# Performance work log

Measured on AMD Instinct MI355X. Metric: run time of the kernel, lower is better.

Reference implementation:

```python
import jax, jax.numpy as jnp
import numpy as np

N_NODES = 100000
EMB_DIM = 64
HIDDEN = 8
OUT_DIM = 16
NUM_HEADS = 3
B = 1024
E_RAND = 3200000


def setup_inputs() -> dict:
    key = jax.random.key(0)
    ks = jax.random.split(key, 12)
    src = jax.random.randint(ks[0], (E_RAND,), 0, N_NODES, dtype=jnp.int32)
    dst = jax.random.randint(ks[1], (E_RAND,), 0, N_NODES, dtype=jnp.int32)
    loop = jnp.arange(N_NODES, dtype=jnp.int32)
    src = jnp.concatenate([src, loop])
    dst = jnp.concatenate([dst, loop])
    # multi-hot query indicator, ~50 items per query, guarantee >=1 item
    queries = (jax.random.uniform(ks[2], (B, N_NODES)) < 5e-4).astype(jnp.float32)
    queries = queries.at[:, 0].set(1.0)
    pos_items = jax.random.randint(ks[3], (B,), 0, N_NODES, dtype=jnp.int32)
    neg_items = jax.random.randint(ks[4], (B,), 0, N_NODES, dtype=jnp.int32)
    embedding = jax.random.normal(ks[5], (N_NODES, EMB_DIM), dtype=jnp.float32) * 0.1
    # GAT layer 1: NUM_HEADS heads, in=64 -> out=8 per head (concat)
    W1 = jax.random.normal(ks[6], (NUM_HEADS, EMB_DIM, HIDDEN), dtype=jnp.float32) * 0.1
    a1 = jax.random.normal(ks[7], (NUM_HEADS, 2 * HIDDEN), dtype=jnp.float32) * 0.1
    # GAT layer 2: 1 head, in=24 -> out=16
    W2 = jax.random.normal(ks[8], (NUM_HEADS * HIDDEN, OUT_DIM), dtype=jnp.float32) * 0.1
    a2 = jax.random.normal(ks[9], (2 * OUT_DIM,), dtype=jnp.float32) * 0.1
    return {"queries": queries, "pos_items": pos_items, "neg_items": neg_items,
            "embedding": embedding, "W1": W1, "a1": a1, "W2": W2, "a2": a2,
            "src": src, "dst": dst}


def gat_layer(h, W, a, src, dst, n_nodes):
    # h: [N, in], W: [H, in, o], a: [H, 2o]; returns [N, H, o]
    o = W.shape[-1]
    z = jnp.einsum('nd,hdo->nho', h, W)            # [N,H,o]
    zs, zd = z[src], z[dst]                         # [E,H,o]
    e = jax.nn.leaky_relu(
        jnp.einsum('eho,ho->eh', zs, a[:, :o]) +
        jnp.einsum('eho,ho->eh', zd, a[:, o:]), 0.01)  # [E,H]
    m = jax.ops.segment_max(e, dst, num_segments=n_nodes)       # [N,H]
    alpha = jnp.exp(e - m[dst])                                  # [E,H]
    denom = jax.ops.segment_sum(alpha, dst, num_segments=n_nodes)
    num = jax.ops.segment_sum(alpha[:, :, None] * zs, dst, num_segments=n_nodes)
    return num / denom[:, :, None]


def gat_forward(embedding, W1, a1, W2, a2, src, dst):
    n = embedding.shape[0]
    h1 = gat_layer(embedding, W1, a1, src, dst, n)       # [N,H,hid]
    h1 = jax.nn.elu(h1.reshape(n, -1))                   # [N,H*hid]
    h2 = gat_layer(h1, W2[None], a2[None], src, dst, n)  # [N,1,out]
    return h2[:, 0]                                      # [N,out]


def reference(queries, pos_items, neg_items, embedding, W1, a1, W2, a2, src, dst):
    item_embeds = gat_forward(embedding, W1, a1, W2, a2, src, dst)  # [N,16]
    item_cnt = jnp.sum(queries, axis=1)                              # [B]
    query_embeds = jnp.matmul(queries, item_embeds) / item_cnt[:, None]
    pos_embed = item_embeds[pos_items]
    neg_embed = item_embeds[neg_items]
    return (query_embeds, pos_embed, neg_embed)
```

## Files before the change

### kernel.cpp

```cpp
#include <hip/hip_runtime.h>
#include <hip/hip_fp16.h>

#define NH 3
#define HID 8
#define C1 24
#define C2 16
#define BSH 5
#define BNODES 32
#define NBMAX 3200
#define SCAP 1792
#define PCHUNK 32768
#define AZS 32

__device__ inline float2 cvt2(unsigned u) {
    __half2 h;
    *reinterpret_cast<unsigned*>(&h) = u;
    return __half22float2(h);
}

__global__ __launch_bounds__(256) void k_z1(
    const float* __restrict__ emb, const float* __restrict__ W1g,
    const float* __restrict__ a1g, __half* __restrict__ az1h,
    float4* __restrict__ f1d, int* __restrict__ bcnt, int NB, int N) {
    __shared__ float sW[NH * 64 * HID];
    __shared__ float sa[NH * 2 * HID];
    for (int i = threadIdx.x; i < NH * 64 * HID; i += blockDim.x) sW[i] = W1g[i];
    for (int i = threadIdx.x; i < NH * 2 * HID; i += blockDim.x) sa[i] = a1g[i];
    int n = blockIdx.x * blockDim.x + threadIdx.x;
    if (n < NB) bcnt[n] = 0;
    __syncthreads();
    if (n >= N) return;
    float e[64];
    const float4* ep = (const float4*)(emb + (size_t)n * 64);
#pragma unroll
    for (int i = 0; i < 16; ++i) {
        float4 v = ep[i];
        e[4*i+0] = v.x; e[4*i+1] = v.y; e[4*i+2] = v.z; e[4*i+3] = v.w;
    }
    float z[C1];
#pragma unroll
    for (int c = 0; c < C1; ++c) z[c] = 0.f;
    for (int d = 0; d < 64; ++d) {
        float ed = e[d];
#pragma unroll
        for (int h = 0; h < NH; ++h) {
            const float4* wp = (const float4*)&sW[(h * 64 + d) * HID];
            float4 w0 = wp[0], w1 = wp[1];
            z[h*HID+0] += ed * w0.x; z[h*HID+1] += ed * w0.y;
            z[h*HID+2] += ed * w0.z; z[h*HID+3] += ed * w0.w;
            z[h*HID+4] += ed * w1.x; z[h*HID+5] += ed * w1.y;
            z[h*HID+6] += ed * w1.z; z[h*HID+7] += ed * w1.w;
        }
    }
    float fs[NH], fd[NH];
#pragma unroll
    for (int h = 0; h < NH; ++h) {
        float s = 0.f, dsum = 0.f;
#pragma unroll
        for (int o = 0; o < HID; ++o) {
            s    += z[h*HID+o] * sa[h*2*HID + o];
            dsum += z[h*HID+o] * sa[h*2*HID + HID + o];
        }
        fs[h] = s; fd[h] = dsum;
    }
    __half hb[32];
    hb[0] = __float2half_rn(fs[0]); hb[1] = __float2half_rn(fs[1]);
    hb[2] = __float2half_rn(fs[2]); hb[3] = __half(0.f);
#pragma unroll
    for (int o = 0; o < C1; ++o) hb[4 + o] = __float2half_rn(z[o]);
#pragma unroll
    for (int o = 28; o < 32; ++o) hb[o] = __half(0.f);
    uint4* zo = (uint4*)(az1h + ((size_t)n << 5));
    const uint4* hbu = (const uint4*)hb;
    zo[0] = hbu[0]; zo[1] = hbu[1]; zo[2] = hbu[2]; zo[3] = hbu[3];
    f1d[n] = make_float4(fd[0], fd[1], fd[2], 0.f);
}

__global__ __launch_bounds__(256) void k_count(const int* __restrict__ dst,
                                               int* __restrict__ bcnt, int E, int NB) {
    __shared__ int lh[NBMAX];
    for (int i = threadIdx.x; i < NB; i += 256) lh[i] = 0;
    __syncthreads();
    int base = blockIdx.x * PCHUNK;
    int end = base + PCHUNK; if (end > E) end = E;
    for (int i = base + threadIdx.x; i < end; i += 256)
        atomicAdd(&lh[dst[i] >> BSH], 1);
    __syncthreads();
    for (int i = threadIdx.x; i < NB; i += 256)
        if (lh[i]) atomicAdd(&bcnt[i], lh[i]);
}

#define SCANK 13
__global__ __launch_bounds__(256) void k_bscan(const int* __restrict__ bcnt,
                                               int* __restrict__ boff,
                                               int* __restrict__ bcur,
                                               int* __restrict__ rowptr,
                                               int NB, int N, int E) {
    __shared__ int sd[256];
    int tid = threadIdx.x;
    int v[SCANK]; int tsum = 0;
#pragma unroll
    for (int i = 0; i < SCANK; ++i) {
        int g = tid * SCANK + i;
        v[i] = (g < NB) ? bcnt[g] : 0;
        tsum += v[i];
    }
    sd[tid] = tsum; __syncthreads();
    for (int off = 1; off < 256; off <<= 1) {
        int t = (tid >= off) ? sd[tid - off] : 0;
        __syncthreads();
        sd[tid] += t;
        __syncthreads();
    }
    int pref = sd[tid] - tsum;
#pragma unroll
    for (int i = 0; i < SCANK; ++i) {
        int g = tid * SCANK + i;
        if (g < NB) { boff[g] = pref; bcur[g] = pref; pref += v[i]; }
    }
    if (tid == 255) boff[NB] = pref;
    if (tid == 0) rowptr[N] = E;
}

__global__ __launch_bounds__(256) void k_part(const int* __restrict__ src,
                                              const int* __restrict__ dst,
                                              int* __restrict__ bcur,
                                              int* __restrict__ bedges, int E, int NB) {
    __shared__ int lh[NBMAX];
    __shared__ int lbase[NBMAX];
    for (int i = threadIdx.x; i < NB; i += 256) lh[i] = 0;
    __syncthreads();
    int base = blockIdx.x * PCHUNK;
    int end = base + PCHUNK; if (end > E) end = E;
    for (int i = base + threadIdx.x; i < end; i += 256)
        atomicAdd(&lh[dst[i] >> BSH], 1);
    __syncthreads();
    for (int i = threadIdx.x; i < NB; i += 256) {
        int c = lh[i];
        lbase[i] = c ? atomicAdd(&bcur[i], c) : 0;
        lh[i] = 0;
    }
    __syncthreads();
    for (int i = base + threadIdx.x; i < end; i += 256) {
        int d = dst[i];
        int b = d >> BSH;
        int p = lbase[b] + atomicAdd(&lh[b], 1);
        bedges[p] = src[i] | ((d & (BNODES - 1)) << 17);
    }
}

__global__ __launch_bounds__(256) void k_gat1(
    const int* __restrict__ boff, int* __restrict__ bedges,
    const __half* __restrict__ az1h, const float4* __restrict__ f1d,
    const float* __restrict__ W2g, const float* __restrict__ a2g,
    __half* __restrict__ z2h, float* __restrict__ f2s, float* __restrict__ f2d,
    int* __restrict__ rowptr, int N) {
    __shared__ int ssrc[SCAP];
    __shared__ int scnt[BNODES];
    __shared__ int sstart[BNODES + 1];
    __shared__ int scur[BNODES];
    __shared__ float sW2[C1 * C2];
    __shared__ float sa2[2 * C2];
    int tid = threadIdx.x;
    int b = blockIdx.x;
    int beg = boff[b], cnt = boff[b + 1] - beg;
    if (tid < BNODES) scnt[tid] = 0;
    for (int i = tid; i < C1 * C2; i += 256) sW2[i] = W2g[i];
    if (tid < 2 * C2) sa2[tid] = a2g[tid];
    __syncthreads();
    for (int i = tid; i < cnt; i += 256)
        atomicAdd(&scnt[bedges[beg + i] >> 17], 1);
    __syncthreads();
    if (tid < BNODES) {
        int v = scnt[tid];
        int x = v;
        for (int d = 1; d < BNODES; d <<= 1) {
            int t = __shfl_up(x, d, 64);
            if (tid >= d) x += t;
        }
        sstart[tid] = x - v;
        scur[tid] = x - v;
        if (tid == BNODES - 1) sstart[BNODES] = x;
    }
    __syncthreads();
    for (int i = tid; i < cnt; i += 256) {
        int pk = bedges[beg + i];
        int p = atomicAdd(&scur[pk >> 17], 1);
        ssrc[p] = pk & 0x1FFFF;
    }
    __syncthreads();
    for (int i = tid; i < cnt; i += 256) bedges[beg + i] = ssrc[i];
    int n0 = b << BSH;
    if (tid < BNODES) rowptr[n0 + tid] = beg + sstart[tid];
    int nl = tid >> 3, l8 = tid & 7;
    int n = n0 + nl;
    int s0 = sstart[nl], s1 = sstart[nl + 1];
    float4 fdv = (n < N) ? f1d[n] : make_float4(0.f, 0.f, 0.f, 0.f);
    float acc[C1];
#pragma unroll
    for (int c = 0; c < C1; ++c) acc[c] = 0.f;
    float den0 = 0.f, den1 = 0.f, den2 = 0.f;
    for (int i = s0 + l8; i < s1; i += 8) {
        int s = ssrc[i];
        const uint4* up = (const uint4*)(az1h + ((size_t)s << 5));
        uint4 u0 = up[0], u1 = up[1], u2 = up[2], u3 = up[3];
        float2 p01 = cvt2(u0.x), p2x = cvt2(u0.y);
        float e0 = p01.x + fdv.x, e1 = p01.y + fdv.y, e2 = p2x.x + fdv.z;
        e0 = e0 > 0.f ? e0 : 0.01f * e0;
        e1 = e1 > 0.f ? e1 : 0.01f * e1;
        e2 = e2 > 0.f ? e2 : 0.01f * e2;
        float a0 = __expf(e0), a1 = __expf(e1), a2v = __expf(e2);
        den0 += a0; den1 += a1; den2 += a2v;
        float2 z0 = cvt2(u0.z), z1 = cvt2(u0.w);
        float2 z2v = cvt2(u1.x), z3 = cvt2(u1.y), z4 = cvt2(u1.z), z5 = cvt2(u1.w);
        float2 z6 = cvt2(u2.x), z7 = cvt2(u2.y), z8 = cvt2(u2.z), z9 = cvt2(u2.w);
        float2 z10 = cvt2(u3.x), z11 = cvt2(u3.y);
        acc[0]  += a0 * z0.x;  acc[1]  += a0 * z0.y;
        acc[2]  += a0 * z1.x;  acc[3]  += a0 * z1.y;
        acc[4]  += a0 * z2v.x; acc[5]  += a0 * z2v.y;
        acc[6]  += a0 * z3.x;  acc[7]  += a0 * z3.y;
        acc[8]  += a1 * z4.x;  acc[9]  += a1 * z4.y;
        acc[10] += a1 * z5.x;  acc[11] += a1 * z5.y;
        acc[12] += a1 * z6.x;  acc[13] += a1 * z6.y;
        acc[14] += a1 * z7.x;  acc[15] += a1 * z7.y;
        acc[16] += a2v * z8.x;  acc[17] += a2v * z8.y;
        acc[18] += a2v * z9.x;  acc[19] += a2v * z9.y;
        acc[20] += a2v * z10.x; acc[21] += a2v * z10.y;
        acc[22] += a2v * z11.x; acc[23] += a2v * z11.y;
    }
#pragma unroll
    for (int c = 0; c < C1; ++c) {
        acc[c] += __shfl_xor(acc[c], 1, 64);
        acc[c] += __shfl_xor(acc[c], 2, 64);
        acc[c] += __shfl_xor(acc[c], 4, 64);
    }
    den0 += __shfl_xor(den0, 1, 64); den0 += __shfl_xor(den0, 2, 64); den0 += __shfl_xor(den0, 4, 64);
    den1 += __shfl_xor(den1, 1, 64); den1 += __shfl_xor(den1, 2, 64); den1 += __shfl_xor(den1, 4, 64);
    den2 += __shfl_xor(den2, 1, 64); den2 += __shfl_xor(den2, 2, 64); den2 += __shfl_xor(den2, 4, 64);
    if (l8 == 0 && n < N) {
        float h1v[C1];
        float inv0 = 1.f / den0, inv1 = 1.f / den1, inv2 = 1.f / den2;
#pragma unroll
        for (int o = 0; o < HID; ++o) {
            float v0 = acc[o] * inv0;
            float v1 = acc[HID + o] * inv1;
            float v2 = acc[2 * HID + o] * inv2;
            h1v[o]           = v0 > 0.f ? v0 : (__expf(v0) - 1.f);
            h1v[HID + o]     = v1 > 0.f ? v1 : (__expf(v1) - 1.f);
            h1v[2 * HID + o] = v2 > 0.f ? v2 : (__expf(v2) - 1.f);
        }
        float zz[C2];
#pragma unroll
        for (int k = 0; k < C2; ++k) zz[k] = 0.f;
        for (int c = 0; c < C1; ++c) {
            float hv = h1v[c];
#pragma unroll
            for (int k = 0; k < C2; ++k) zz[k] += hv * sW2[c * C2 + k];
        }
        float fs = 0.f, fdd = 0.f;
#pragma unroll
        for (int k = 0; k < C2; ++k) {
            fs  += zz[k] * sa2[k];
            fdd += zz[k] * sa2[C2 + k];
        }
        __half zb[16];
#pragma unroll
        for (int k = 0; k < C2; ++k) zb[k] = __float2half_rn(zz[k]);
        uint4* zo = (uint4*)(z2h + ((size_t)n << 4));
        const uint4* zbu = (const uint4*)zb;
        zo[0] = zbu[0]; zo[1] = zbu[1];
        f2s[n] = fs;
        f2d[n] = fdd;
    }
}

__global__ __launch_bounds__(256) void k_gat2(
    const int* __restrict__ rowptr, const int* __restrict__ csr,
    const __half* __restrict__ z2h, const float* __restrict__ f2s,
    const float* __restrict__ f2d, float* __restrict__ item, int N) {
    int t = blockIdx.x * blockDim.x + threadIdx.x;
    int n = t >> 3, l8 = t & 7;
    if (n >= N) return;
    int beg = rowptr[n], end = rowptr[n + 1];
    float fdv = f2d[n];
    float acc[C2];
#pragma unroll
    for (int k = 0; k < C2; ++k) acc[k] = 0.f;
    float den = 0.f;
    for (int i = beg + l8; i < end; i += 8) {
        int s = csr[i];
        float e = f2s[s] + fdv;
        e = e > 0.f ? e : 0.01f * e;
        float a = __expf(e);
        den += a;
        const uint4* zp = (const uint4*)(z2h + ((size_t)s << 4));
        uint4 u0 = zp[0], u1 = zp[1];
        float2 z0 = cvt2(u0.x), z1 = cvt2(u0.y), z2v = cvt2(u0.z), z3 = cvt2(u0.w);
        float2 z4 = cvt2(u1.x), z5 = cvt2(u1.y), z6 = cvt2(u1.z), z7 = cvt2(u1.w);
        acc[0]  += a * z0.x;  acc[1]  += a * z0.y;
        acc[2]  += a * z1.x;  acc[3]  += a * z1.y;
        acc[4]  += a * z2v.x; acc[5]  += a * z2v.y;
        acc[6]  += a * z3.x;  acc[7]  += a * z3.y;
        acc[8]  += a * z4.x;  acc[9]  += a * z4.y;
        acc[10] += a * z5.x;  acc[11] += a * z5.y;
        acc[12] += a * z6.x;  acc[13] += a * z6.y;
        acc[14] += a * z7.x;  acc[15] += a * z7.y;
    }
#pragma unroll
    for (int k = 0; k < C2; ++k) {
        acc[k] += __shfl_xor(acc[k], 1, 64);
        acc[k] += __shfl_xor(acc[k], 2, 64);
        acc[k] += __shfl_xor(acc[k], 4, 64);
    }
    den += __shfl_xor(den, 1, 64);
    den += __shfl_xor(den, 2, 64);
    den += __shfl_xor(den, 4, 64);
    if (l8 == 0) {
        float inv = 1.f / den;
        float4* io = (float4*)(item + (size_t)n * C2);
#pragma unroll
        for (int i = 0; i < 4; ++i)
            io[i] = make_float4(acc[4*i]*inv, acc[4*i+1]*inv, acc[4*i+2]*inv, acc[4*i+3]*inv);
    }
}

__global__ __launch_bounds__(256) void k_query(
    const float* __restrict__ queries, const float* __restrict__ item,
    const int* __restrict__ pos, const int* __restrict__ neg,
    float* __restrict__ out, int N, int B) {
    int b = blockIdx.x;
    const float4* qrow = (const float4*)(queries + (size_t)b * N);
    int n4 = N >> 2;
    float acc[C2];
#pragma unroll
    for (int k = 0; k < C2; ++k) acc[k] = 0.f;
    float cnt = 0.f;
    for (int i = threadIdx.x; i < n4; i += 256) {
        float4 v = qrow[i];
        int j = i * 4;
        float vv[4] = {v.x, v.y, v.z, v.w};
#pragma unroll
        for (int c = 0; c < 4; ++c) {
            if (vv[c] != 0.f) {
                cnt += vv[c];
                const float4* rp = (const float4*)(item + (size_t)(j + c) * C2);
                float4 r0 = rp[0], r1 = rp[1], r2 = rp[2], r3 = rp[3];
                acc[0]  += vv[c]*r0.x; acc[1]  += vv[c]*r0.y; acc[2]  += vv[c]*r0.z; acc[3]  += vv[c]*r0.w;
                acc[4]  += vv[c]*r1.x; acc[5]  += vv[c]*r1.y; acc[6]  += vv[c]*r1.z; acc[7]  += vv[c]*r1.w;
                acc[8]  += vv[c]*r2.x; acc[9]  += vv[c]*r2.y; acc[10] += vv[c]*r2.z; acc[11] += vv[c]*r2.w;
                acc[12] += vv[c]*r3.x; acc[13] += vv[c]*r3.y; acc[14] += vv[c]*r3.z; acc[15] += vv[c]*r3.w;
            }
        }
    }
    int rem = N & 3;
    if ((int)threadIdx.x < rem) {
        int j = n4 * 4 + threadIdx.x;
        float qv = queries[(size_t)b * N + j];
        if (qv != 0.f) {
            cnt += qv;
#pragma unroll
            for (int k = 0; k < C2; ++k) acc[k] += qv * item[(size_t)j * C2 + k];
        }
    }
    __shared__ float red[4][C2 + 1];
    int lane = threadIdx.x & 63, wid = threadIdx.x >> 6;
#pragma unroll
    for (int k = 0; k < C2; ++k)
        for (int off = 32; off; off >>= 1) acc[k] += __shfl_down(acc[k], off, 64);
    for (int off = 32; off; off >>= 1) cnt += __shfl_down(cnt, off, 64);
    if (lane == 0) {
#pragma unroll
        for (int k = 0; k < C2; ++k) red[wid][k] = acc[k];
        red[wid][C2] = cnt;
    }
    __syncthreads();
    if (threadIdx.x < C2 + 1) {
        float s = red[0][threadIdx.x] + red[1][threadIdx.x] +
                  red[2][threadIdx.x] + red[3][threadIdx.x];
        red[0][threadIdx.x] = s;
    }
    __syncthreads();
    if (threadIdx.x < C2)
        out[(size_t)b * C2 + threadIdx.x] = red[0][threadIdx.x] / red[0][C2];
    else if (threadIdx.x >= 64 && threadIdx.x < 64 + C2)
        out[((size_t)B + b) * C2 + (threadIdx.x - 64)] =
            item[(size_t)pos[b] * C2 + (threadIdx.x - 64)];
    else if (threadIdx.x >= 128 && threadIdx.x < 128 + C2)
        out[((size_t)2 * B + b) * C2 + (threadIdx.x - 128)] =
            item[(size_t)neg[b] * C2 + (threadIdx.x - 128)];
}

extern "C" void kernel_launch(void* const* d_in, const int* in_sizes, int n_in,
                              void* d_out, int out_size, void* d_ws, size_t ws_size,
                              hipStream_t stream) {
    const float* queries = (const float*)d_in[0];
    const int*   pos     = (const int*)d_in[1];
    const int*   neg     = (const int*)d_in[2];
    const float* emb     = (const float*)d_in[3];
    const float* W1      = (const float*)d_in[4];
    const float* a1      = (const float*)d_in[5];
    const float* W2      = (const float*)d_in[6];
    const float* a2      = (const float*)d_in[7];
    const int*   src     = (const int*)d_in[8];
    const int*   dst     = (const int*)d_in[9];

    int B = in_sizes[1];
    int N = in_sizes[3] / 64;
    int E = in_sizes[8];
    float* out = (float*)d_out;

    int NB = (N + BNODES - 1) >> BSH;

    char* w = (char*)d_ws;
    auto alloc = [&](size_t bytes) -> char* {
        char* p = w;
        w += (bytes + 255) & ~(size_t)255;
        return p;
    };
    __half* az1h   = (__half*)alloc(sizeof(__half) * (size_t)N * AZS);
    float4* f1d    = (float4*)alloc(sizeof(float4) * (size_t)N);
    __half* z2h    = (__half*)alloc(sizeof(__half) * (size_t)N * C2);
    float*  f2s    = (float*)alloc(sizeof(float) * (size_t)N);
    float*  f2d    = (float*)alloc(sizeof(float) * (size_t)N);
    float*  item   = (float*)alloc(sizeof(float) * (size_t)N * C2);
    int*    bcnt   = (int*)alloc(sizeof(int) * (size_t)NB);
    int*    boff   = (int*)alloc(sizeof(int) * (size_t)(NB + 1));
    int*    bcur   = (int*)alloc(sizeof(int) * (size_t)NB);
    int*    rowptr = (int*)alloc(sizeof(int) * (size_t)(N + 1));
    int*    bedges = (int*)alloc(sizeof(int) * (size_t)E);

    int nblkN = (N + 255) / 256;
    int nPart = (E + PCHUNK - 1) / PCHUNK;

    k_z1<<<nblkN, 256, 0, stream>>>(emb, W1, a1, az1h, f1d, bcnt, NB, N);
    k_count<<<nPart, 256, 0, stream>>>(dst, bcnt, E, NB);
    k_bscan<<<1, 256, 0, stream>>>(bcnt, boff, bcur, rowptr, NB, N, E);
    k_part<<<nPart, 256, 0, stream>>>(src, dst, bcur, bedges, E, NB);
    k_gat1<<<NB, 256, 0, stream>>>(boff, bedges, az1h, f1d, W2, a2,
                                   z2h, f2s, f2d, rowptr, N);
    k_gat2<<<(N * 8 + 255) / 256, 256, 0, stream>>>(rowptr, bedges, z2h, f2s, f2d, item, N);
    k_query<<<B, 256, 0, stream>>>(queries, item, pos, neg, out, N, B);
}
```

Measured before the change: 893.5 us.

## Split per-edge feature loads across lanes in both GAT aggregation kernels

In both GAT aggregation kernels, each edge's source row is now spread over several lanes: 4 lanes each load one 16-byte quarter of the row in layer 1, and 2 lanes each load half in layer 2. Before, one lane loaded the whole row, so each lane now does fewer loads, keeps fewer accumulators and needs a shorter shuffle reduction. Layer 1 broadcasts the attention coefficients with shuffles and gathers the partial sums in shared memory behind an extra barrier before the final layer-2 projection. In exchange, only 2 edges per node are processed in parallel in layer 1 instead of 8, and 4 instead of 8 in layer 2. The n<N guard on the f1d load is also dropped.

```diff
diff --git a/kernel.cpp b/kernel.cpp
--- a/kernel.cpp
+++ b/kernel.cpp
@@ -161,6 +161,7 @@
     __shared__ int scur[BNODES];
     __shared__ float sW2[C1 * C2];
     __shared__ float sa2[2 * C2];
+    __shared__ float sagg[BNODES * 28];
     int tid = threadIdx.x;
     int b = blockIdx.x;
     int beg = boff[b], cnt = boff[b + 1] - beg;
@@ -192,59 +193,71 @@
     for (int i = tid; i < cnt; i += 256) bedges[beg + i] = ssrc[i];
     int n0 = b << BSH;
     if (tid < BNODES) rowptr[n0 + tid] = beg + sstart[tid];
-    int nl = tid >> 3, l8 = tid & 7;
+
+    int nl = tid >> 3;
+    int g  = (tid >> 2) & 1;
+    int q  = tid & 3;
+    int lane = tid & 63;
+    int base4 = lane & ~3;
     int n = n0 + nl;
     int s0 = sstart[nl], s1 = sstart[nl + 1];
-    float4 fdv = (n < N) ? f1d[n] : make_float4(0.f, 0.f, 0.f, 0.f);
-    float acc[C1];
-#pragma unroll
-    for (int c = 0; c < C1; ++c) acc[c] = 0.f;
+    float4 fdv = f1d[n];
+    float accLo[4], accHi[4];
+#pragma unroll
+    for (int j = 0; j < 4; ++j) { accLo[j] = 0.f; accHi[j] = 0.f; }
     float den0 = 0.f, den1 = 0.f, den2 = 0.f;
-    for (int i = s0 + l8; i < s1; i += 8) {
+    bool q1f = (q == 1), q2f = (q == 2), q3f = (q == 3), q0f = (q == 0);
+    for (int i = s0 + g; i < s1; i += 2) {
         int s = ssrc[i];
-        const uint4* up = (const uint4*)(az1h + ((size_t)s << 5));
-        uint4 u0 = up[0], u1 = up[1], u2 = up[2], u3 = up[3];
-        float2 p01 = cvt2(u0.x), p2x = cvt2(u0.y);
-        float e0 = p01.x + fdv.x, e1 = p01.y + fdv.y, e2 = p2x.x + fdv.z;
+        uint4 u = *((const uint4*)(az1h + ((size_t)s << 5)) + q);
+        float2 v0 = cvt2(u.x), v1 = cvt2(u.y), v2 = cvt2(u.z), v3 = cvt2(u.w);
+        float e0 = v0.x + fdv.x, e1 = v0.y + fdv.y, e2 = v1.x + fdv.z;
         e0 = e0 > 0.f ? e0 : 0.01f * e0;
         e1 = e1 > 0.f ? e1 : 0.01f * e1;
         e2 = e2 > 0.f ? e2 : 0.01f * e2;
-        float a0 = __expf(e0), a1 = __expf(e1), a2v = __expf(e2);
-        den0 += a0; den1 += a1; den2 += a2v;
-        float2 z0 = cvt2(u0.z), z1 = cvt2(u0.w);
-        float2 z2v = cvt2(u1.x), z3 = cvt2(u1.y), z4 = cvt2(u1.z), z5 = cvt2(u1.w);
-        float2 z6 = cvt2(u2.x), z7 = cvt2(u2.y), z8 = cvt2(u2.z), z9 = cvt2(u2.w);
-        float2 z10 = cvt2(u3.x), z11 = cvt2(u3.y);
-        acc[0]  += a0 * z0.x;  acc[1]  += a0 * z0.y;
-        acc[2]  += a0 * z1.x;  acc[3]  += a0 * z1.y;
-        acc[4]  += a0 * z2v.x; acc[5]  += a0 * z2v.y;
-        acc[6]  += a0 * z3.x;  acc[7]  += a0 * z3.y;
-        acc[8]  += a1 * z4.x;  acc[9]  += a1 * z4.y;
-        acc[10] += a1 * z5.x;  acc[11] += a1 * z5.y;
-        acc[12] += a1 * z6.x;  acc[13] += a1 * z6.y;
-        acc[14] += a1 * z7.x;  acc[15] += a1 * z7.y;
-        acc[16] += a2v * z8.x;  acc[17] += a2v * z8.y;
-        acc[18] += a2v * z9.x;  acc[19] += a2v * z9.y;
-        acc[20] += a2v * z10.x; acc[21] += a2v * z10.y;
-        acc[22] += a2v * z11.x; acc[23] += a2v * z11.y;
-    }
-#pragma unroll
-    for (int c = 0; c < C1; ++c) {
-        acc[c] += __shfl_xor(acc[c], 1, 64);
-        acc[c] += __shfl_xor(acc[c], 2, 64);
-        acc[c] += __shfl_xor(acc[c], 4, 64);
-    }
-    den0 += __shfl_xor(den0, 1, 64); den0 += __shfl_xor(den0, 2, 64); den0 += __shfl_xor(den0, 4, 64);
-    den1 += __shfl_xor(den1, 1, 64); den1 += __shfl_xor(den1, 2, 64); den1 += __shfl_xor(den1, 4, 64);
-    den2 += __shfl_xor(den2, 1, 64); den2 += __shfl_xor(den2, 2, 64); den2 += __shfl_xor(den2, 4, 64);
-    if (l8 == 0 && n < N) {
+        float a0 = __expf(e0), a1 = __expf(e1), a2 = __expf(e2);
+        float b0 = __shfl(a0, base4, 64);
+        float b1 = __shfl(a1, base4, 64);
+        float b2 = __shfl(a2, base4, 64);
+        den0 += b0; den1 += b1; den2 += b2;
+        float cLo = q1f ? b0 : (q2f ? b1 : (q3f ? b2 : 0.f));
+        float cHi = q0f ? b0 : (q1f ? b1 : (q2f ? b2 : 0.f));
+        accLo[0] += cLo * v0.x; accLo[1] += cLo * v0.y;
+        accLo[2] += cLo * v1.x; accLo[3] += cLo * v1.y;
+        accHi[0] += cHi * v2.x; accHi[1] += cHi * v2.y;
+        accHi[2] += cHi * v3.x; accHi[3] += cHi * v3.y;
+    }
+#pragma unroll
+    for (int j = 0; j < 4; ++j) {
+        accLo[j] += __shfl_xor(accLo[j], 4, 64);
+        accHi[j] += __shfl_xor(accHi[j], 4, 64);
+    }
+    den0 += __shfl_xor(den0, 4, 64);
+    den1 += __shfl_xor(den1, 4, 64);
+    den2 += __shfl_xor(den2, 4, 64);
+    if (g == 0) {
+        float* sg = &sagg[nl * 28];
+        if (q > 0) {
+#pragma unroll
+            for (int j = 0; j < 4; ++j) sg[q * 8 - 4 + j] = accLo[j];
+        }
+        if (q < 3) {
+#pragma unroll
+            for (int j = 0; j < 4; ++j) sg[q * 8 + j] = accHi[j];
+        }
+        if (q == 0) { sg[24] = den0; sg[25] = den1; sg[26] = den2; }
+    }
+    __syncthreads();
+    if (tid < BNODES) {
+        const float* sg = &sagg[tid * 28];
+        int nn = n0 + tid;
         float h1v[C1];
-        float inv0 = 1.f / den0, inv1 = 1.f / den1, inv2 = 1.f / den2;
+        float inv0 = 1.f / sg[24], inv1 = 1.f / sg[25], inv2 = 1.f / sg[26];
 #pragma unroll
         for (int o = 0; o < HID; ++o) {
-            float v0 = acc[o] * inv0;
-            float v1 = acc[HID + o] * inv1;
-            float v2 = acc[2 * HID + o] * inv2;
+            float v0 = sg[o] * inv0;
+            float v1 = sg[HID + o] * inv1;
+            float v2 = sg[2 * HID + o] * inv2;
             h1v[o]           = v0 > 0.f ? v0 : (__expf(v0) - 1.f);
             h1v[HID + o]     = v1 > 0.f ? v1 : (__expf(v1) - 1.f);
             h1v[2 * HID + o] = v2 > 0.f ? v2 : (__expf(v2) - 1.f);
@@ -266,11 +279,11 @@
         __half zb[16];
 #pragma unroll
         for (int k = 0; k < C2; ++k) zb[k] = __float2half_rn(zz[k]);
-        uint4* zo = (uint4*)(z2h + ((size_t)n << 4));
+        uint4* zo = (uint4*)(z2h + ((size_t)nn << 4));
         const uint4* zbu = (const uint4*)zb;
         zo[0] = zbu[0]; zo[1] = zbu[1];
-        f2s[n] = fs;
-        f2d[n] = fdd;
+        f2s[nn] = fs;
+        f2d[nn] = fdd;
     }
 }
 
@@ -279,48 +292,41 @@
     const __half* __restrict__ z2h, const float* __restrict__ f2s,
     const float* __restrict__ f2d, float* __restrict__ item, int N) {
     int t = blockIdx.x * blockDim.x + threadIdx.x;
-    int n = t >> 3, l8 = t & 7;
+    int n = t >> 3;
     if (n >= N) return;
+    int q  = t & 1;
+    int g  = (t >> 1) & 3;
     int beg = rowptr[n], end = rowptr[n + 1];
     float fdv = f2d[n];
-    float acc[C2];
-#pragma unroll
-    for (int k = 0; k < C2; ++k) acc[k] = 0.f;
+    float acc[8];
+#pragma unroll
+    for (int j = 0; j < 8; ++j) acc[j] = 0.f;
     float den = 0.f;
-    for (int i = beg + l8; i < end; i += 8) {
+    for (int i = beg + g; i < end; i += 4) {
         int s = csr[i];
         float e = f2s[s] + fdv;
         e = e > 0.f ? e : 0.01f * e;
         float a = __expf(e);
         den += a;
-        const uint4* zp = (const uint4*)(z2h + ((size_t)s << 4));
-        uint4 u0 = zp[0], u1 = zp[1];
-        float2 z0 = cvt2(u0.x), z1 = cvt2(u0.y), z2v = cvt2(u0.z), z3 = cvt2(u0.w);
-        float2 z4 = cvt2(u1.x), z5 = cvt2(u1.y), z6 = cvt2(u1.z), z7 = cvt2(u1.w);
-        acc[0]  += a * z0.x;  acc[1]  += a * z0.y;
-        acc[2]  += a * z1.x;  acc[3]  += a * z1.y;
-        acc[4]  += a * z2v.x; acc[5]  += a * z2v.y;
-        acc[6]  += a * z3.x;  acc[7]  += a * z3.y;
-        acc[8]  += a * z4.x;  acc[9]  += a * z4.y;
-        acc[10] += a * z5.x;  acc[11] += a * z5.y;
-        acc[12] += a * z6.x;  acc[13] += a * z6.y;
-        acc[14] += a * z7.x;  acc[15] += a * z7.y;
-    }
-#pragma unroll
-    for (int k = 0; k < C2; ++k) {
-        acc[k] += __shfl_xor(acc[k], 1, 64);
-        acc[k] += __shfl_xor(acc[k], 2, 64);
-        acc[k] += __shfl_xor(acc[k], 4, 64);
-    }
-    den += __shfl_xor(den, 1, 64);
+        uint4 u = *((const uint4*)(z2h + ((size_t)s << 4)) + q);
+        float2 v0 = cvt2(u.x), v1 = cvt2(u.y), v2 = cvt2(u.z), v3 = cvt2(u.w);
+        acc[0] += a * v0.x; acc[1] += a * v0.y;
+        acc[2] += a * v1.x; acc[3] += a * v1.y;
+        acc[4] += a * v2.x; acc[5] += a * v2.y;
+        acc[6] += a * v3.x; acc[7] += a * v3.y;
+    }
+#pragma unroll
+    for (int j = 0; j < 8; ++j) {
+        acc[j] += __shfl_xor(acc[j], 2, 64);
+        acc[j] += __shfl_xor(acc[j], 4, 64);
+    }
     den += __shfl_xor(den, 2, 64);
     den += __shfl_xor(den, 4, 64);
-    if (l8 == 0) {
+    if ((t & 6) == 0) {
         float inv = 1.f / den;
-        float4* io = (float4*)(item + (size_t)n * C2);
-#pragma unroll
-        for (int i = 0; i < 4; ++i)
-            io[i] = make_float4(acc[4*i]*inv, acc[4*i+1]*inv, acc[4*i+2]*inv, acc[4*i+3]*inv);
+        float4* io = (float4*)(item + (size_t)n * C2 + q * 8);
+        io[0] = make_float4(acc[0]*inv, acc[1]*inv, acc[2]*inv, acc[3]*inv);
+        io[1] = make_float4(acc[4]*inv, acc[5]*inv, acc[6]*inv, acc[7]*inv);
     }
 }
 
```

After: 892.4 us. No clear change (-0.1%).
